# Kernel optimization log

Hardware: AMD Instinct MI355X
Metric: run time of the kernel (lower is better)

The kernel has to match this reference:

```python
import jax, jax.numpy as jnp
import numpy as np

B, T, D, DV = 4, 4096, 1024, 4
K_EPS = 1e-05
V_SIG_SCALE = 4.0


def setup_inputs() -> dict:
    key = jax.random.key(0)
    ks = jax.random.split(key, 8)
    x = jax.random.normal(ks[0], (B, T, D, DV), dtype=jnp.float32)
    k_in = jax.random.normal(ks[1], (B, T, D), dtype=jnp.float32)
    v_in = jax.random.normal(ks[2], (B, T, D), dtype=jnp.float32)
    context = jax.random.normal(ks[3], (B, T, D), dtype=jnp.float32)
    # small learned linears (PyTorch Linear: y = x @ W.T + b)
    beta_w = jax.random.normal(ks[4], (1, D), dtype=jnp.float32) / np.sqrt(D)
    beta_b = jnp.full((1,), -13.8155, dtype=jnp.float32)  # logit(1e-6) init
    v_w = jax.random.normal(ks[5], (DV, D), dtype=jnp.float32) / np.sqrt(D)
    v_b = jnp.zeros((DV,), dtype=jnp.float32)
    return {"x": x, "k_in": k_in, "v_in": v_in, "context": context,
            "beta_w": beta_w, "beta_b": beta_b, "v_w": v_w, "v_b": v_b}


def reference(x, k_in, v_in, context, beta_w, beta_b, v_w, v_b):
    k_dim = k_in.shape[-1]
    eps_rms = (K_EPS * K_EPS) / float(k_dim)
    k_scale = 1.0 / np.sqrt(float(k_dim)).astype(np.float32)
    # RMSNorm over feature dim (no learned gain), matching F.rms_norm
    ms = jnp.mean(jnp.square(k_in), axis=-1, keepdims=True)
    k_rms = k_in * jax.lax.rsqrt(ms + eps_rms)                     # (B,T,D)
    # beta gate: single linear -> 2*sigmoid, in float32
    beta_logits = (jnp.einsum('btd,od->bto', context, beta_w) + beta_b).astype(jnp.float32)
    beta = 2.0 * jax.nn.sigmoid(beta_logits)                       # (B,T,1)
    # reduction contraction over feature dim, accumulated in float32
    proj = jnp.einsum('btd,btdv->btv', k_rms.astype(jnp.float32),
                      x.astype(jnp.float32)) * k_scale             # (B,T,DV)
    # v gate: small linear -> sigmoid * scale
    v = jax.nn.sigmoid(jnp.einsum('btd,vd->btv', v_in, v_w) + v_b) * V_SIG_SCALE
    delta_row = beta * (v - proj) * k_scale                        # (B,T,DV) fp32
    # outer-product delta update broadcast back into the state tensor
    update = k_rms[..., :, None] * delta_row.astype(x.dtype)[..., None, :]
    return x + update
```

## Files before the change

kernel.cpp:

```cpp
#include <hip/hip_runtime.h>
#include <math.h>

#define DIMD 1024
#define DIMV 4
#define NROWS 16384
#define K_SCALE 0.03125f
#define EPS_RMS (1e-10f / 1024.0f)
#define V_SIG_SCALE 4.0f

typedef float f32x4 __attribute__((ext_vector_type(4)));

__global__ __launch_bounds__(256) void ddre_kernel(
    const float* __restrict__ x,
    const float* __restrict__ k_in,
    const float* __restrict__ v_in,
    const float* __restrict__ context,
    const float* __restrict__ beta_w,
    const float* __restrict__ beta_b,
    const float* __restrict__ v_w,
    const float* __restrict__ v_b,
    float* __restrict__ out)
{
    const int tid  = threadIdx.x;
    const int wave = tid >> 6;
    const int lane = tid & 63;
    const int row  = (blockIdx.x << 2) | wave;

    const float* xrow = x    + (size_t)row * (DIMD * DIMV);
    const float* krow = k_in + (size_t)row * DIMD;

    f32x4 xr[16];
    #pragma unroll
    for (int j = 0; j < 16; ++j)
        xr[j] = __builtin_nontemporal_load(
                    (const f32x4*)(xrow + (size_t)(lane + 64 * j) * DIMV));

    float kr[16];
    #pragma unroll
    for (int j = 0; j < 16; ++j)
        kr[j] = krow[lane + 64 * j];

    const float* crow = context + (size_t)row * DIMD;
    const float* vrow = v_in    + (size_t)row * DIMD;
    float s_ctx = 0.0f;
    float s_v0 = 0.0f, s_v1 = 0.0f, s_v2 = 0.0f, s_v3 = 0.0f;
    #pragma unroll
    for (int m = 0; m < 4; ++m) {
        const int off = 4 * lane + 256 * m;
        const float4 c  = *(const float4*)(crow   + off);
        const float4 b  = *(const float4*)(beta_w + off);
        s_ctx += c.x*b.x + c.y*b.y + c.z*b.z + c.w*b.w;
        const float4 vv = *(const float4*)(vrow + off);
        const float4 w0 = *(const float4*)(v_w + 0 * DIMD + off);
        const float4 w1 = *(const float4*)(v_w + 1 * DIMD + off);
        const float4 w2 = *(const float4*)(v_w + 2 * DIMD + off);
        const float4 w3 = *(const float4*)(v_w + 3 * DIMD + off);
        s_v0 += vv.x*w0.x + vv.y*w0.y + vv.z*w0.z + vv.w*w0.w;
        s_v1 += vv.x*w1.x + vv.y*w1.y + vv.z*w1.z + vv.w*w1.w;
        s_v2 += vv.x*w2.x + vv.y*w2.y + vv.z*w2.z + vv.w*w2.w;
        s_v3 += vv.x*w3.x + vv.y*w3.y + vv.z*w3.z + vv.w*w3.w;
    }

    float s_k2 = 0.0f;
    float sx = 0.0f, sy = 0.0f, sz = 0.0f, sw = 0.0f;
    #pragma unroll
    for (int j = 0; j < 16; ++j) {
        s_k2 += kr[j] * kr[j];
        sx += kr[j] * xr[j].x;
        sy += kr[j] * xr[j].y;
        sz += kr[j] * xr[j].z;
        sw += kr[j] * xr[j].w;
    }

    float s[10] = {s_k2, s_ctx, s_v0, s_v1, s_v2, s_v3, sx, sy, sz, sw};
    #pragma unroll
    for (int i = 0; i < 10; ++i) {
        #pragma unroll
        for (int off = 32; off >= 1; off >>= 1)
            s[i] += __shfl_xor(s[i], off, 64);
    }

    const float ms   = s[0] * (1.0f / (float)DIMD);
    const float rinv = rsqrtf(ms + EPS_RMS);
    const float beta = 2.0f / (1.0f + expf(-(s[1] + beta_b[0])));

    float delta[4];
    delta[0] = beta * (V_SIG_SCALE / (1.0f + expf(-(s[2] + v_b[0]))) - s[6] * rinv * K_SCALE) * K_SCALE;
    delta[1] = beta * (V_SIG_SCALE / (1.0f + expf(-(s[3] + v_b[1]))) - s[7] * rinv * K_SCALE) * K_SCALE;
    delta[2] = beta * (V_SIG_SCALE / (1.0f + expf(-(s[4] + v_b[2]))) - s[8] * rinv * K_SCALE) * K_SCALE;
    delta[3] = beta * (V_SIG_SCALE / (1.0f + expf(-(s[5] + v_b[3]))) - s[9] * rinv * K_SCALE) * K_SCALE;

    float* orow = out + (size_t)row * (DIMD * DIMV);
    #pragma unroll
    for (int j = 0; j < 16; ++j) {
        const float krms = kr[j] * rinv;
        f32x4 o;
        o.x = xr[j].x + krms * delta[0];
        o.y = xr[j].y + krms * delta[1];
        o.z = xr[j].z + krms * delta[2];
        o.w = xr[j].w + krms * delta[3];
        __builtin_nontemporal_store(o,
            (f32x4*)(orow + (size_t)(lane + 64 * j) * DIMV));
    }
}

extern "C" void kernel_launch(void* const* d_in, const int* in_sizes, int n_in,
                              void* d_out, int out_size, void* d_ws, size_t ws_size,
                              hipStream_t stream) {
    const float* x       = (const float*)d_in[0];
    const float* k_in    = (const float*)d_in[1];
    const float* v_in    = (const float*)d_in[2];
    const float* context = (const float*)d_in[3];
    const float* beta_w  = (const float*)d_in[4];
    const float* beta_b  = (const float*)d_in[5];
    const float* v_w     = (const float*)d_in[6];
    const float* v_b     = (const float*)d_in[7];
    float* out = (float*)d_out;

    ddre_kernel<<<NROWS / 4, 256, 0, stream>>>(x, k_in, v_in, context,
                                               beta_w, beta_b, v_w, v_b, out);
}
```

Baseline: 110.3 us.

## Split each row across two waves with shared-memory partial-sum exchange

Each row is now handled by two waves that each cover half of the feature dimension, so the grid doubles and each thread holds half as many x and k registers. The per-wave partial sums are combined through shared memory and a block barrier before the gates and the delta are computed. The goal is lower register pressure and more memory-level parallelism, so the memory-bound stream runs at higher occupancy. The cost is an added __syncthreads, a shared-memory round trip, and twice as many blocks.

```diff
diff --git a/kernel.cpp b/kernel.cpp
--- a/kernel.cpp
+++ b/kernel.cpp
@@ -24,29 +24,31 @@
     const int tid  = threadIdx.x;
     const int wave = tid >> 6;
     const int lane = tid & 63;
-    const int row  = (blockIdx.x << 2) | wave;
+    const int half = wave & 1;
+    const int row  = (blockIdx.x << 1) | (wave >> 1);
 
     const float* xrow = x    + (size_t)row * (DIMD * DIMV);
     const float* krow = k_in + (size_t)row * DIMD;
+    const int dbase = (half << 9) + lane;
 
-    f32x4 xr[16];
+    f32x4 xr[8];
     #pragma unroll
-    for (int j = 0; j < 16; ++j)
+    for (int j = 0; j < 8; ++j)
         xr[j] = __builtin_nontemporal_load(
-                    (const f32x4*)(xrow + (size_t)(lane + 64 * j) * DIMV));
+                    (const f32x4*)(xrow + (size_t)(dbase + 64 * j) * DIMV));
 
-    float kr[16];
+    float kr[8];
     #pragma unroll
-    for (int j = 0; j < 16; ++j)
-        kr[j] = krow[lane + 64 * j];
+    for (int j = 0; j < 8; ++j)
+        kr[j] = krow[dbase + 64 * j];
 
     const float* crow = context + (size_t)row * DIMD;
     const float* vrow = v_in    + (size_t)row * DIMD;
     float s_ctx = 0.0f;
     float s_v0 = 0.0f, s_v1 = 0.0f, s_v2 = 0.0f, s_v3 = 0.0f;
     #pragma unroll
-    for (int m = 0; m < 4; ++m) {
-        const int off = 4 * lane + 256 * m;
+    for (int m = 0; m < 2; ++m) {
+        const int off = 4 * lane + 256 * ((half << 1) + m);
         const float4 c  = *(const float4*)(crow   + off);
         const float4 b  = *(const float4*)(beta_w + off);
         s_ctx += c.x*b.x + c.y*b.y + c.z*b.z + c.w*b.w;
@@ -64,7 +66,7 @@
     float s_k2 = 0.0f;
     float sx = 0.0f, sy = 0.0f, sz = 0.0f, sw = 0.0f;
     #pragma unroll
-    for (int j = 0; j < 16; ++j) {
+    for (int j = 0; j < 8; ++j) {
         s_k2 += kr[j] * kr[j];
         sx += kr[j] * xr[j].x;
         sy += kr[j] * xr[j].y;
@@ -80,19 +82,30 @@
             s[i] += __shfl_xor(s[i], off, 64);
     }
 
-    const float ms   = s[0] * (1.0f / (float)DIMD);
+    __shared__ float red[4][10];
+    if (lane == 0) {
+        #pragma unroll
+        for (int i = 0; i < 10; ++i) red[wave][i] = s[i];
+    }
+    __syncthreads();
+    const int partner = wave ^ 1;
+    float t[10];
+    #pragma unroll
+    for (int i = 0; i < 10; ++i) t[i] = s[i] + red[partner][i];
+
+    const float ms   = t[0] * (1.0f / (float)DIMD);
     const float rinv = rsqrtf(ms + EPS_RMS);
-    const float beta = 2.0f / (1.0f + expf(-(s[1] + beta_b[0])));
+    const float beta = 2.0f / (1.0f + expf(-(t[1] + beta_b[0])));
 
     float delta[4];
-    delta[0] = beta * (V_SIG_SCALE / (1.0f + expf(-(s[2] + v_b[0]))) - s[6] * rinv * K_SCALE) * K_SCALE;
-    delta[1] = beta * (V_SIG_SCALE / (1.0f + expf(-(s[3] + v_b[1]))) - s[7] * rinv * K_SCALE) * K_SCALE;
-    delta[2] = beta * (V_SIG_SCALE / (1.0f + expf(-(s[4] + v_b[2]))) - s[8] * rinv * K_SCALE) * K_SCALE;
-    delta[3] = beta * (V_SIG_SCALE / (1.0f + expf(-(s[5] + v_b[3]))) - s[9] * rinv * K_SCALE) * K_SCALE;
+    delta[0] = beta * (V_SIG_SCALE / (1.0f + expf(-(t[2] + v_b[0]))) - t[6] * rinv * K_SCALE) * K_SCALE;
+    delta[1] = beta * (V_SIG_SCALE / (1.0f + expf(-(t[3] + v_b[1]))) - t[7] * rinv * K_SCALE) * K_SCALE;
+    delta[2] = beta * (V_SIG_SCALE / (1.0f + expf(-(t[4] + v_b[2]))) - t[8] * rinv * K_SCALE) * K_SCALE;
+    delta[3] = beta * (V_SIG_SCALE / (1.0f + expf(-(t[5] + v_b[3]))) - t[9] * rinv * K_SCALE) * K_SCALE;
 
     float* orow = out + (size_t)row * (DIMD * DIMV);
     #pragma unroll
-    for (int j = 0; j < 16; ++j) {
+    for (int j = 0; j < 8; ++j) {
         const float krms = kr[j] * rinv;
         f32x4 o;
         o.x = xr[j].x + krms * delta[0];
@@ -100,7 +113,7 @@
         o.z = xr[j].z + krms * delta[2];
         o.w = xr[j].w + krms * delta[3];
         __builtin_nontemporal_store(o,
-            (f32x4*)(orow + (size_t)(lane + 64 * j) * DIMV));
+            (f32x4*)(orow + (size_t)(dbase + 64 * j) * DIMV));
     }
 }
 
@@ -117,6 +130,6 @@
     const float* v_b     = (const float*)d_in[7];
     float* out = (float*)d_out;
 
-    ddre_kernel<<<NROWS / 4, 256, 0, stream>>>(x, k_in, v_in, context,
+    ddre_kernel<<<NROWS / 2, 256, 0, stream>>>(x, k_in, v_in, context,
                                                beta_w, beta_b, v_w, v_b, out);
 }
```

After: 111.6 us. About the same (+1.1%).
